# Optimization experiments

Measured on AMD Instinct MI355X. Metric: run time of the kernel, lower is better.

The kernel has to match this reference:

```python
import jax, jax.numpy as jnp
import numpy as np

LAMDA = 1.0  # init arg: weight on uniformity term
ALIGN_ALPHA = 2.0
UNIF_T = 2.0
EPS = 1e-12


def _l2_normalize(x):
    # F.normalize(x, dim=1): x / max(||x||, eps)
    n = jnp.sqrt(jnp.sum(x * x, axis=1, keepdims=True))
    return x / jnp.maximum(n, EPS)


def _lalign(q, k):
    # mean over batch of ||q_i - k_i||_2 ^ alpha (alpha=2 -> squared distance)
    d2 = jnp.sum((q - k) ** 2, axis=1)
    return jnp.mean(d2)


def _lunif(x):
    # log( mean_{i<j} exp(-t * ||x_i - x_j||^2) )
    # x is unit-norm, so ||x_i - x_j||^2 = 2 - 2 <x_i, x_j>
    n = x.shape[0]
    sq = jnp.maximum(2.0 - 2.0 * (x @ x.T), 0.0)            # [N, N] squared dists
    iu = jnp.triu(jnp.ones((n, n), dtype=bool), k=1)        # strict upper: i < j pairs
    vals = jnp.where(iu, jnp.exp(-UNIF_T * sq), 0.0)
    npairs = jnp.asarray(n * (n - 1) // 2, dtype=x.dtype)
    return jnp.log(vals.sum() / npairs)


def setup_inputs() -> dict:
    key = jax.random.key(0)
    kq, kk = jax.random.split(key)
    q = jax.random.normal(kq, (8192, 128), dtype=jnp.float32)
    k = jax.random.normal(kk, (8192, 128), dtype=jnp.float32)
    return {"q": q, "k": k}


def reference(q, k):
    qn = _l2_normalize(q)
    kn = _l2_normalize(k)
    align = _lalign(qn, kn)
    uniform = (_lunif(qn) + _lunif(kn)) / 2.0
    return align + LAMDA * uniform
```

## Files before the change

kernel.cpp:

```cpp
#include <hip/hip_runtime.h>
#include <math.h>

#define NROWS 8192
#define DIM   128
#define NT    64
#define TRI   2080

typedef __attribute__((ext_vector_type(8))) __bf16 bf16x8;
typedef __attribute__((ext_vector_type(4))) float  f32x4;

__device__ __forceinline__ unsigned short f2bf(float f) {
    unsigned int u = __float_as_uint(f);
    u += 0x7fffu + ((u >> 16) & 1u);
    return (unsigned short)(u >> 16);
}

__global__ __launch_bounds__(256) void norm_kernel(
        const float* __restrict__ q, const float* __restrict__ k,
        unsigned int* __restrict__ qn, unsigned int* __restrict__ kn,
        float* __restrict__ align_part) {
    int wave = threadIdx.x >> 6;
    int lane = threadIdx.x & 63;
    int row  = blockIdx.x * 4 + wave;

    const float2 qv = reinterpret_cast<const float2*>(q)[row * 64 + lane];
    const float2 kv = reinterpret_cast<const float2*>(k)[row * 64 + lane];

    float sq = qv.x * qv.x + qv.y * qv.y;
    float sk = kv.x * kv.x + kv.y * kv.y;
    #pragma unroll
    for (int off = 32; off; off >>= 1) {
        sq += __shfl_xor(sq, off);
        sk += __shfl_xor(sk, off);
    }
    float qi = 1.0f / fmaxf(sqrtf(sq), 1e-12f);
    float ki = 1.0f / fmaxf(sqrtf(sk), 1e-12f);
    float qx = qv.x * qi, qy = qv.y * qi;
    float kx = kv.x * ki, ky = kv.y * ki;

    qn[row * 64 + lane] = (unsigned int)f2bf(qx) | ((unsigned int)f2bf(qy) << 16);
    kn[row * 64 + lane] = (unsigned int)f2bf(kx) | ((unsigned int)f2bf(ky) << 16);

    float dx = qx - kx, dy = qy - ky;
    float d2 = dx * dx + dy * dy;
    #pragma unroll
    for (int off = 32; off; off >>= 1) d2 += __shfl_xor(d2, off);

    __shared__ float red[4];
    if (lane == 0) red[wave] = d2;
    __syncthreads();
    if (threadIdx.x == 0)
        align_part[blockIdx.x] = red[0] + red[1] + red[2] + red[3];
}

__global__ __launch_bounds__(256) void gram_kernel(
        const uint4* __restrict__ qn, const uint4* __restrict__ kn,
        float* __restrict__ unif_part) {
    __shared__ uint4 lds[4096];
    __shared__ float red[4];

    int bid = blockIdx.x;
    int mat = 0, t = bid;
    if (t >= TRI) { mat = 1; t -= TRI; }
    int ti = 0, rem = t;
    while (rem >= NT - ti) { rem -= NT - ti; ++ti; }
    int tj = ti + rem;
    const uint4* __restrict__ x = mat ? kn : qn;

    int tid = threadIdx.x;
    {
        int s = tid & 15;
        int rb = tid >> 4;
        #pragma unroll
        for (int it = 0; it < 8; ++it) {
            int r = it * 16 + rb;
            int sw = s ^ (r & 7);
            lds[r * 16 + sw]        = x[(ti * 128 + r) * 16 + s];
            lds[2048 + r * 16 + sw] = x[(tj * 128 + r) * 16 + s];
        }
    }
    __syncthreads();

    int wid = tid >> 6, lane = tid & 63;
    int wr = wid >> 1, wc = wid & 1;
    int lr = lane & 15, lg = lane >> 4;

    f32x4 c[4][4];
    #pragma unroll
    for (int m = 0; m < 4; ++m)
        #pragma unroll
        for (int n = 0; n < 4; ++n)
            c[m][n] = (f32x4){0.f, 0.f, 0.f, 0.f};

    #pragma unroll
    for (int ks = 0; ks < 4; ++ks) {
        int slot = ks * 4 + lg;
        bf16x8 a[4], b[4];
        #pragma unroll
        for (int m = 0; m < 4; ++m) {
            int r = wr * 64 + m * 16 + lr;
            a[m] = *reinterpret_cast<const bf16x8*>(&lds[r * 16 + (slot ^ (r & 7))]);
        }
        #pragma unroll
        for (int n = 0; n < 4; ++n) {
            int r = wc * 64 + n * 16 + lr;
            b[n] = *reinterpret_cast<const bf16x8*>(&lds[2048 + r * 16 + (slot ^ (r & 7))]);
        }
        #pragma unroll
        for (int m = 0; m < 4; ++m)
            #pragma unroll
            for (int n = 0; n < 4; ++n)
                c[m][n] = __builtin_amdgcn_mfma_f32_16x16x32_bf16(a[m], b[n], c[m][n], 0, 0, 0);
    }

    const float C1 = 4.0f * 1.4426950408889634f;
    const float C0 = -4.0f * 1.4426950408889634f;
    bool diag = (ti == tj);
    float psum = 0.0f;
    int crow0 = wr * 64 + lg * 4;
    int ccol0 = wc * 64 + lr;
    #pragma unroll
    for (int m = 0; m < 4; ++m)
        #pragma unroll
        for (int n = 0; n < 4; ++n)
            #pragma unroll
            for (int r = 0; r < 4; ++r) {
                float g = c[m][n][r];
                float w = fminf(fmaf(g, C1, C0), 0.0f);
                float e = exp2f(w);
                if (diag) {
                    int lrow = crow0 + m * 16 + r;
                    int lcol = ccol0 + n * 16;
                    e = (lcol > lrow) ? e : 0.0f;
                }
                psum += e;
            }
    #pragma unroll
    for (int off = 32; off; off >>= 1) psum += __shfl_xor(psum, off);

    if (lane == 0) red[wid] = psum;
    __syncthreads();
    if (tid == 0)
        unif_part[bid] = red[0] + red[1] + red[2] + red[3];
}

__global__ __launch_bounds__(256) void finalize(
        const float* __restrict__ align_part,
        const float* __restrict__ unif_part,
        float* __restrict__ out) {
    int tid = threadIdx.x;
    double a = 0.0, qs = 0.0, ks = 0.0;
    for (int i = tid; i < 2048; i += 256) a  += (double)align_part[i];
    for (int i = tid; i < TRI;  i += 256) qs += (double)unif_part[i];
    for (int i = tid; i < TRI;  i += 256) ks += (double)unif_part[TRI + i];

    __shared__ double sa[256], sq[256], sk[256];
    sa[tid] = a; sq[tid] = qs; sk[tid] = ks;
    __syncthreads();
    for (int s = 128; s; s >>= 1) {
        if (tid < s) {
            sa[tid] += sa[tid + s];
            sq[tid] += sq[tid + s];
            sk[tid] += sk[tid + s];
        }
        __syncthreads();
    }
    if (tid == 0) {
        const double npairs = (double)NROWS * (NROWS - 1) / 2.0;
        double align = sa[0] / (double)NROWS;
        double lq = log(sq[0] / npairs);
        double lk = log(sk[0] / npairs);
        out[0] = (float)(align + 0.5 * (lq + lk));
    }
}

extern "C" void kernel_launch(void* const* d_in, const int* in_sizes, int n_in,
                              void* d_out, int out_size, void* d_ws, size_t ws_size,
                              hipStream_t stream) {
    const float* q = (const float*)d_in[0];
    const float* k = (const float*)d_in[1];
    char* ws = (char*)d_ws;
    unsigned int* qn = (unsigned int*)ws;
    unsigned int* kn = (unsigned int*)(ws + (size_t)2 * 1024 * 1024);
    float* align_part = (float*)(ws + (size_t)4 * 1024 * 1024);
    float* unif_part  = (float*)(ws + (size_t)4 * 1024 * 1024 + 16384);
    float* out = (float*)d_out;

    norm_kernel<<<NROWS / 4, 256, 0, stream>>>(q, k, qn, kn, align_part);
    gram_kernel<<<2 * TRI, 256, 0, stream>>>((const uint4*)qn, (const uint4*)kn, unif_part);
    finalize<<<1, 256, 0, stream>>>(align_part, unif_part, out);
}
```

Measured before the change: 111.7 us.

## Use 8 waves per Gram tile and vectorize off-diagonal exp epilogue

The Gram kernel now runs 512 threads per 128x128 tile in a 2x4 wave grid, so each wave computes a 64x32 subtile instead of 64x64, halving accumulator registers and spreading the exp epilogue over more waves. Off-diagonal tiles get a separate epilogue with no clamp and no mask, written with packed float2 FMA so the compiler can use packed ops. The aim is more parallelism and latency hiding in the exp-heavy epilogue. The cost is more LDS A-fragment rereads per tile and a larger block reduction. Dropping the clamp changes results only by rounding, since unit-norm dot products stay at or below one.

```diff
diff --git a/kernel.cpp b/kernel.cpp
--- a/kernel.cpp
+++ b/kernel.cpp
@@ -8,6 +8,7 @@
 
 typedef __attribute__((ext_vector_type(8))) __bf16 bf16x8;
 typedef __attribute__((ext_vector_type(4))) float  f32x4;
+typedef __attribute__((ext_vector_type(2))) float  f32x2;
 
 __device__ __forceinline__ unsigned short f2bf(float f) {
     unsigned int u = __float_as_uint(f);
@@ -53,11 +54,11 @@
         align_part[blockIdx.x] = red[0] + red[1] + red[2] + red[3];
 }
 
-__global__ __launch_bounds__(256) void gram_kernel(
+__global__ __launch_bounds__(512) void gram_kernel(
         const uint4* __restrict__ qn, const uint4* __restrict__ kn,
         float* __restrict__ unif_part) {
     __shared__ uint4 lds[4096];
-    __shared__ float red[4];
+    __shared__ float red[8];
 
     int bid = blockIdx.x;
     int mat = 0, t = bid;
@@ -72,8 +73,8 @@
         int s = tid & 15;
         int rb = tid >> 4;
         #pragma unroll
-        for (int it = 0; it < 8; ++it) {
-            int r = it * 16 + rb;
+        for (int it = 0; it < 4; ++it) {
+            int r = it * 32 + rb;
             int sw = s ^ (r & 7);
             lds[r * 16 + sw]        = x[(ti * 128 + r) * 16 + s];
             lds[2048 + r * 16 + sw] = x[(tj * 128 + r) * 16 + s];
@@ -82,66 +83,87 @@
     __syncthreads();
 
     int wid = tid >> 6, lane = tid & 63;
-    int wr = wid >> 1, wc = wid & 1;
+    int wr = wid >> 2, wc = wid & 3;
     int lr = lane & 15, lg = lane >> 4;
 
-    f32x4 c[4][4];
+    f32x4 c[4][2];
     #pragma unroll
     for (int m = 0; m < 4; ++m)
         #pragma unroll
-        for (int n = 0; n < 4; ++n)
+        for (int n = 0; n < 2; ++n)
             c[m][n] = (f32x4){0.f, 0.f, 0.f, 0.f};
 
     #pragma unroll
     for (int ks = 0; ks < 4; ++ks) {
         int slot = ks * 4 + lg;
-        bf16x8 a[4], b[4];
+        bf16x8 a[4], b[2];
         #pragma unroll
         for (int m = 0; m < 4; ++m) {
             int r = wr * 64 + m * 16 + lr;
             a[m] = *reinterpret_cast<const bf16x8*>(&lds[r * 16 + (slot ^ (r & 7))]);
         }
         #pragma unroll
-        for (int n = 0; n < 4; ++n) {
-            int r = wc * 64 + n * 16 + lr;
+        for (int n = 0; n < 2; ++n) {
+            int r = wc * 32 + n * 16 + lr;
             b[n] = *reinterpret_cast<const bf16x8*>(&lds[2048 + r * 16 + (slot ^ (r & 7))]);
         }
         #pragma unroll
         for (int m = 0; m < 4; ++m)
             #pragma unroll
-            for (int n = 0; n < 4; ++n)
+            for (int n = 0; n < 2; ++n)
                 c[m][n] = __builtin_amdgcn_mfma_f32_16x16x32_bf16(a[m], b[n], c[m][n], 0, 0, 0);
     }
 
     const float C1 = 4.0f * 1.4426950408889634f;
     const float C0 = -4.0f * 1.4426950408889634f;
     bool diag = (ti == tj);
-    float psum = 0.0f;
-    int crow0 = wr * 64 + lg * 4;
-    int ccol0 = wc * 64 + lr;
-    #pragma unroll
-    for (int m = 0; m < 4; ++m)
-        #pragma unroll
-        for (int n = 0; n < 4; ++n)
+    float psum;
+    if (!diag) {
+        f32x2 acc2 = (f32x2){0.f, 0.f};
+        #pragma unroll
+        for (int m = 0; m < 4; ++m)
             #pragma unroll
-            for (int r = 0; r < 4; ++r) {
-                float g = c[m][n][r];
-                float w = fminf(fmaf(g, C1, C0), 0.0f);
-                float e = exp2f(w);
-                if (diag) {
+            for (int n = 0; n < 2; ++n) {
+                f32x4 g = c[m][n];
+                f32x2 glo = (f32x2){g[0], g[1]};
+                f32x2 ghi = (f32x2){g[2], g[3]};
+                f32x2 wlo = glo * C1 + C0;
+                f32x2 whi = ghi * C1 + C0;
+                f32x2 elo = (f32x2){exp2f(wlo.x), exp2f(wlo.y)};
+                f32x2 ehi = (f32x2){exp2f(whi.x), exp2f(whi.y)};
+                acc2 += elo;
+                acc2 += ehi;
+            }
+        psum = acc2.x + acc2.y;
+    } else {
+        psum = 0.0f;
+        int crow0 = wr * 64 + lg * 4;
+        int ccol0 = wc * 32 + lr;
+        #pragma unroll
+        for (int m = 0; m < 4; ++m)
+            #pragma unroll
+            for (int n = 0; n < 2; ++n)
+                #pragma unroll
+                for (int r = 0; r < 4; ++r) {
+                    float g = c[m][n][r];
+                    float w = fminf(fmaf(g, C1, C0), 0.0f);
+                    float e = exp2f(w);
                     int lrow = crow0 + m * 16 + r;
                     int lcol = ccol0 + n * 16;
-                    e = (lcol > lrow) ? e : 0.0f;
+                    psum += (lcol > lrow) ? e : 0.0f;
                 }
-                psum += e;
-            }
+    }
     #pragma unroll
     for (int off = 32; off; off >>= 1) psum += __shfl_xor(psum, off);
 
     if (lane == 0) red[wid] = psum;
     __syncthreads();
-    if (tid == 0)
-        unif_part[bid] = red[0] + red[1] + red[2] + red[3];
+    if (tid == 0) {
+        float s = 0.0f;
+        #pragma unroll
+        for (int w = 0; w < 8; ++w) s += red[w];
+        unif_part[bid] = s;
+    }
 }
 
 __global__ __launch_bounds__(256) void finalize(
@@ -187,6 +209,6 @@
     float* out = (float*)d_out;
 
     norm_kernel<<<NROWS / 4, 256, 0, stream>>>(q, k, qn, kn, align_part);
-    gram_kernel<<<2 * TRI, 256, 0, stream>>>((const uint4*)qn, (const uint4*)kn, unif_part);
+    gram_kernel<<<2 * TRI, 512, 0, stream>>>((const uint4*)qn, (const uint4*)kn, unif_part);
     finalize<<<1, 256, 0, stream>>>(align_part, unif_part, out);
 }
```

New measurement: 106.8 us. 4.4% less time.

## Load gram tiles directly to LDS and use bit-trick exp approximation

Applied to the files above, without the earlier changes.

Gram tile loads now use global_load_lds, which writes straight into LDS without passing through VGPRs, and the swizzle widens to 16 slots. The exp2 in the epilogue is replaced by a Schraudolph-style approximation that converts a scaled float to int and reinterprets it as a float. Off-diagonal tiles skip the min-clamp and use packed f32x2 arithmetic. The approximate exp trades accuracy for fewer transcendental instructions, and dropping the clamp off the diagonal assumes dot products never exceed 1.

```diff
diff --git a/kernel.cpp b/kernel.cpp
--- a/kernel.cpp
+++ b/kernel.cpp
@@ -8,11 +8,21 @@
 
 typedef __attribute__((ext_vector_type(8))) __bf16 bf16x8;
 typedef __attribute__((ext_vector_type(4))) float  f32x4;
+typedef __attribute__((ext_vector_type(2))) float  f32x2;
 
 __device__ __forceinline__ unsigned short f2bf(float f) {
     unsigned int u = __float_as_uint(f);
     u += 0x7fffu + ((u >> 16) & 1u);
     return (unsigned short)(u >> 16);
+}
+
+__device__ __forceinline__ void gload_lds16(const uint4* g, uint4* l) {
+    __builtin_amdgcn_global_load_lds(
+        (const __attribute__((address_space(1))) uint32_t*)
+            (const __attribute__((address_space(1))) void*)g,
+        (__attribute__((address_space(3))) uint32_t*)
+            (__attribute__((address_space(3))) void*)l,
+        16, 0, 0);
 }
 
 __global__ __launch_bounds__(256) void norm_kernel(
@@ -68,20 +78,23 @@
     const uint4* __restrict__ x = mat ? kn : qn;
 
     int tid = threadIdx.x;
+    int wid = tid >> 6, lane = tid & 63;
+
     {
-        int s = tid & 15;
-        int rb = tid >> 4;
-        #pragma unroll
-        for (int it = 0; it < 8; ++it) {
-            int r = it * 16 + rb;
-            int sw = s ^ (r & 7);
-            lds[r * 16 + sw]        = x[(ti * 128 + r) * 16 + s];
-            lds[2048 + r * 16 + sw] = x[(tj * 128 + r) * 16 + s];
-        }
-    }
-    __syncthreads();
-
-    int wid = tid >> 6, lane = tid & 63;
+        int lrow4 = lane >> 4;
+        int sw    = lane & 15;
+        #pragma unroll
+        for (int it = 0; it < 16; ++it) {
+            int inst = wid * 16 + it;
+            int r    = inst * 4 + lrow4;
+            int rr   = r & 127;
+            int tile = (r < 128) ? ti : tj;
+            int s    = sw ^ (rr & 15);
+            gload_lds16(&x[((size_t)tile * 128 + rr) * 16 + s], &lds[inst * 64]);
+        }
+    }
+    __syncthreads();
+
     int wr = wid >> 1, wc = wid & 1;
     int lr = lane & 15, lg = lane >> 4;
 
@@ -99,12 +112,12 @@
         #pragma unroll
         for (int m = 0; m < 4; ++m) {
             int r = wr * 64 + m * 16 + lr;
-            a[m] = *reinterpret_cast<const bf16x8*>(&lds[r * 16 + (slot ^ (r & 7))]);
+            a[m] = *reinterpret_cast<const bf16x8*>(&lds[r * 16 + (slot ^ (r & 15))]);
         }
         #pragma unroll
         for (int n = 0; n < 4; ++n) {
             int r = wc * 64 + n * 16 + lr;
-            b[n] = *reinterpret_cast<const bf16x8*>(&lds[2048 + r * 16 + (slot ^ (r & 7))]);
+            b[n] = *reinterpret_cast<const bf16x8*>(&lds[2048 + r * 16 + (slot ^ (r & 15))]);
         }
         #pragma unroll
         for (int m = 0; m < 4; ++m)
@@ -113,28 +126,44 @@
                 c[m][n] = __builtin_amdgcn_mfma_f32_16x16x32_bf16(a[m], b[n], c[m][n], 0, 0, 0);
     }
 
-    const float C1 = 4.0f * 1.4426950408889634f;
-    const float C0 = -4.0f * 1.4426950408889634f;
+    const float K1 = 4.0f * 1.4426950408889634f * 8388608.0f;
+    const float B  = 1065353216.0f - 0.05744f * 8388608.0f;
+    const float K0 = B - K1;
     bool diag = (ti == tj);
     float psum = 0.0f;
-    int crow0 = wr * 64 + lg * 4;
-    int ccol0 = wc * 64 + lr;
-    #pragma unroll
-    for (int m = 0; m < 4; ++m)
-        #pragma unroll
-        for (int n = 0; n < 4; ++n)
+    if (!diag) {
+        f32x2 acc2 = (f32x2){0.f, 0.f};
+        #pragma unroll
+        for (int m = 0; m < 4; ++m)
             #pragma unroll
-            for (int r = 0; r < 4; ++r) {
-                float g = c[m][n][r];
-                float w = fminf(fmaf(g, C1, C0), 0.0f);
-                float e = exp2f(w);
-                if (diag) {
+            for (int n = 0; n < 4; ++n) {
+                f32x4 g = c[m][n];
+                f32x2 u0 = (f32x2){g[0], g[1]} * K1 + K0;
+                f32x2 u1 = (f32x2){g[2], g[3]} * K1 + K0;
+                f32x2 e0 = (f32x2){__int_as_float((int)u0.x),
+                                   __int_as_float((int)u0.y)};
+                f32x2 e1 = (f32x2){__int_as_float((int)u1.x),
+                                   __int_as_float((int)u1.y)};
+                acc2 += e0;
+                acc2 += e1;
+            }
+        psum = acc2.x + acc2.y;
+    } else {
+        int crow0 = wr * 64 + lg * 4;
+        int ccol0 = wc * 64 + lr;
+        #pragma unroll
+        for (int m = 0; m < 4; ++m)
+            #pragma unroll
+            for (int n = 0; n < 4; ++n)
+                #pragma unroll
+                for (int r = 0; r < 4; ++r) {
+                    float u = fminf(fmaf(c[m][n][r], K1, K0), B);
+                    float e = __int_as_float((int)u);
                     int lrow = crow0 + m * 16 + r;
                     int lcol = ccol0 + n * 16;
-                    e = (lcol > lrow) ? e : 0.0f;
+                    psum += (lcol > lrow) ? e : 0.0f;
                 }
-                psum += e;
-            }
+    }
     #pragma unroll
     for (int off = 32; off; off >>= 1) psum += __shfl_xor(psum, off);
 
```

Result: faster. 103.2 us (-7.6%).
